# Optimization experiments

Hardware: AMD Instinct MI355X
Metric: run time of the kernel (lower is better)

The kernel has to match this reference:

```python
import jax, jax.numpy as jnp
import numpy as np

MAX_SEQ = 1024
NUM_HEADS = 16
NUM_KV_HEADS = 4
HEAD_DIM = 128
HIDDEN = 2048
GROUPS = NUM_HEADS // NUM_KV_HEADS
EPS = 1e-6
THETA = 1000000.0
SCALE = 1.0 / (HEAD_DIM ** 0.5)
POS = 512
B = 32


def setup_inputs() -> dict:
    key = jax.random.key(0)
    ks = jax.random.split(key, 8)
    x = jax.random.normal(ks[0], (B, 1, HIDDEN), dtype=jnp.float32)
    position = jnp.full((1,), float(POS), dtype=jnp.float32)
    mask = jnp.where(jnp.arange(MAX_SEQ) <= POS, 0.0, -1e9).astype(jnp.float32).reshape(1, 1, 1, MAX_SEQ)
    k_cache = jax.random.normal(ks[1], (B, NUM_KV_HEADS, MAX_SEQ, HEAD_DIM), dtype=jnp.float32)
    v_cache = jax.random.normal(ks[2], (B, NUM_KV_HEADS, MAX_SEQ, HEAD_DIM), dtype=jnp.float32)
    onehot = jnp.zeros((1, 1, MAX_SEQ, 1), dtype=jnp.float32).at[0, 0, POS, 0].set(1.0)
    wq = jax.random.normal(ks[3], (NUM_HEADS * HEAD_DIM, HIDDEN), dtype=jnp.float32) * 0.02
    wk = jax.random.normal(ks[4], (NUM_KV_HEADS * HEAD_DIM, HIDDEN), dtype=jnp.float32) * 0.02
    wv = jax.random.normal(ks[5], (NUM_KV_HEADS * HEAD_DIM, HIDDEN), dtype=jnp.float32) * 0.02
    wo = jax.random.normal(ks[6], (HIDDEN, NUM_HEADS * HEAD_DIM), dtype=jnp.float32) * 0.02
    q_norm_w = jnp.ones((HEAD_DIM,), dtype=jnp.float32)
    k_norm_w = jnp.ones((HEAD_DIM,), dtype=jnp.float32)
    return {"x": x, "position": position, "mask": mask, "k_cache": k_cache, "v_cache": v_cache,
            "onehot": onehot, "wq": wq, "wk": wk, "wv": wv, "wo": wo,
            "q_norm_w": q_norm_w, "k_norm_w": k_norm_w}


def _rmsnorm(t, w):
    tf = t.astype(jnp.float32)
    norm = jax.lax.rsqrt(jnp.mean(tf * tf, axis=-1, keepdims=True) + EPS)
    return (tf * norm * w).astype(t.dtype)


def _rope(t, position):
    half = HEAD_DIM // 2
    inv_freq = 1.0 / (THETA ** (jnp.arange(half, dtype=jnp.float32) / half))
    freqs = position * inv_freq  # [half]
    cos_v = jnp.cos(freqs).reshape(1, 1, 1, half)
    sin_v = jnp.sin(freqs).reshape(1, 1, 1, half)
    x1, x2 = t[..., :half], t[..., half:]
    return jnp.concatenate([x1 * cos_v - x2 * sin_v, x2 * cos_v + x1 * sin_v], axis=-1)


def reference(x, position, mask, k_cache, v_cache, onehot, wq, wk, wv, wo, q_norm_w, k_norm_w):
    Bsz, T, _ = x.shape
    # projections -> [B, heads, T, head_dim]
    q = (x @ wq.T).reshape(Bsz, T, NUM_HEADS, HEAD_DIM).transpose(0, 2, 1, 3)
    k = (x @ wk.T).reshape(Bsz, T, NUM_KV_HEADS, HEAD_DIM).transpose(0, 2, 1, 3)
    v = (x @ wv.T).reshape(Bsz, T, NUM_KV_HEADS, HEAD_DIM).transpose(0, 2, 1, 3)
    q = _rope(_rmsnorm(q, q_norm_w), position)
    k = _rope(_rmsnorm(k, k_norm_w), position)
    # functional one-hot cache update (in-place mul_/add_ in torch)
    kc = k_cache * (1.0 - onehot) + k * onehot  # [B, kvH, MAX_SEQ, hd]
    vc = v_cache * (1.0 - onehot) + v * onehot
    # GQA attention without materializing duplicated K/V: group the query heads
    qg = q.reshape(Bsz, NUM_KV_HEADS, GROUPS, T, HEAD_DIM)
    attn = jnp.einsum('bkgtd,bksd->bkgts', qg, kc) * SCALE  # [B,kvH,G,T,S]
    attn = attn + mask  # mask broadcasts over [*,*,*,T,S]
    attn = jax.nn.softmax(attn, axis=-1)
    out = jnp.einsum('bkgts,bksd->bkgtd', attn, vc)
    out = out.reshape(Bsz, NUM_HEADS, T, HEAD_DIM).transpose(0, 2, 1, 3).reshape(Bsz, T, NUM_HEADS * HEAD_DIM)
    return out @ wo.T
```

## Files before the change

### kernel.cpp

```cpp
#include <hip/hip_runtime.h>
#include <math.h>

#define MAX_SEQ   1024
#define NUM_HEADS 16
#define NUM_KV    4
#define HEAD_DIM  128
#define HIDDEN    2048
#define GROUPS    4
#define EPS       1e-6f
#define THETA     1000000.0f
#define SCALE     0.08838834764831845f
#define NSPLIT    8

#define QBUF  0
#define KBUF  65536
#define VBUF  81920
#define AOUT  98304
#define ARENA 163840

__device__ __forceinline__ void gemv_body(
    const float* __restrict__ W,
    const float* __restrict__ X,
    float* __restrict__ part,
    int RS, int grow0, int nkt)
{
    __shared__ float wt[128 * 68];
    __shared__ float xs[32 * 68];
    const int tid = threadIdx.x, lane = tid & 63, wave = tid >> 6;
    const int rg = tid >> 3, bg = tid & 7;
    const int rrow = wave * 4 + (lane >> 4);
    const int cf = (lane & 15) * 4;

    float acc[4][4];
    #pragma unroll
    for (int i = 0; i < 4; ++i)
        #pragma unroll
        for (int j = 0; j < 4; ++j) acc[i][j] = 0.f;

    for (int kt = 0; kt < nkt; ++kt) {
        const float* Wk = W + kt * 64;
        const float* Xk = X + kt * 64;
        #pragma unroll
        for (int it = 0; it < 8; ++it) {
            const int r = it * 16 + rrow;
            *(float4*)&wt[r * 68 + cf] = *(const float4*)(Wk + (size_t)r * HIDDEN + cf);
        }
        #pragma unroll
        for (int it = 0; it < 2; ++it) {
            const int b = it * 16 + rrow;
            *(float4*)&xs[b * 68 + cf] = *(const float4*)(Xk + (size_t)b * HIDDEN + cf);
        }
        __syncthreads();

        #pragma unroll
        for (int kk = 0; kk < 64; kk += 4) {
            float4 a[4], bb[4];
            #pragma unroll
            for (int i = 0; i < 4; ++i) a[i]  = *(const float4*)&wt[(rg * 4 + i) * 68 + kk];
            #pragma unroll
            for (int j = 0; j < 4; ++j) bb[j] = *(const float4*)&xs[(bg * 4 + j) * 68 + kk];
            #pragma unroll
            for (int i = 0; i < 4; ++i)
                #pragma unroll
                for (int j = 0; j < 4; ++j)
                    acc[i][j] += a[i].x * bb[j].x + a[i].y * bb[j].y
                               + a[i].z * bb[j].z + a[i].w * bb[j].w;
        }
        __syncthreads();
    }

    #pragma unroll
    for (int j = 0; j < 4; ++j) {
        float4 o = make_float4(acc[0][j], acc[1][j], acc[2][j], acc[3][j]);
        *(float4*)(part + (size_t)(bg * 4 + j) * RS + grow0 + rg * 4) = o;
    }
}

__global__ __launch_bounds__(256) void gemv_qkv(
    const float* __restrict__ x, const float* __restrict__ wq,
    const float* __restrict__ wk, const float* __restrict__ wv,
    float* __restrict__ ws)
{
    const int mt = blockIdx.x >> 3;
    const int ks = blockIdx.x & 7;
    const float* W;
    if (mt < 16)      W = wq + (size_t)mt * 128 * HIDDEN;
    else if (mt < 20) W = wk + (size_t)(mt - 16) * 128 * HIDDEN;
    else              W = wv + (size_t)(mt - 20) * 128 * HIDDEN;
    const int k0 = ks * 256;
    float* part = ws + ARENA + (size_t)ks * 32 * 3072;
    gemv_body(W + k0, x + k0, part, 3072, mt * 128, 4);
}

__global__ __launch_bounds__(128) void qkv_post(
    const float* __restrict__ position, const float* __restrict__ qnw,
    const float* __restrict__ knw, float* __restrict__ ws)
{
    const int blk = blockIdx.x;
    const int b = blk / 24, h = blk % 24;
    const int d = threadIdx.x, lane = d & 63, wave = d >> 6;
    const int grow = h * 128 + d;

    float v = 0.f;
    #pragma unroll
    for (int s = 0; s < NSPLIT; ++s)
        v += ws[ARENA + (size_t)(s * 32 + b) * 3072 + grow];

    if (h >= 20) {
        ws[VBUF + (size_t)(b * NUM_KV + (h - 20)) * HEAD_DIM + d] = v;
        return;
    }

    __shared__ float red[2];
    __shared__ float vl[128];
    vl[d] = v;
    float t2 = v * v;
    #pragma unroll
    for (int off = 32; off; off >>= 1) t2 += __shfl_xor(t2, off);
    if (lane == 0) red[wave] = t2;
    __syncthreads();

    if (d < 64) {
        const float norm = rsqrtf((red[0] + red[1]) * (1.0f / HEAD_DIM) + EPS);
        const float* nw = (h < 16) ? qnw : knw;
        float n1 = vl[d]      * norm * nw[d];
        float n2 = vl[d + 64] * norm * nw[d + 64];
        const float p = position[0];
        float invf = __powf(THETA, -(float)d * (1.0f / 64.0f));
        float f = p * invf, s, c;
        __sincosf(f, &s, &c);
        float* outp = (h < 16)
            ? ws + QBUF + (size_t)(b * NUM_HEADS + h) * HEAD_DIM
            : ws + KBUF + (size_t)(b * NUM_KV + (h - 16)) * HEAD_DIM;
        outp[d]      = n1 * c - n2 * s;
        outp[d + 64] = n2 * c + n1 * s;
    }
}

__global__ __launch_bounds__(256) void attn_kernel(
    const float* __restrict__ kcache, const float* __restrict__ vcache,
    const float* __restrict__ position, float* __restrict__ ws)
{
    const int blk = blockIdx.x;
    const int split = blk & (NSPLIT - 1);
    const int bk = blk >> 3;
    const int tid = threadIdx.x, lane = tid & 63, wave = tid >> 6;
    const int half = lane >> 5, li = lane & 31;
    const int b = bk >> 2, kv = bk & 3;
    const int pos = (int)position[0];

    const int chunk = (pos + NSPLIT) / NSPLIT;
    const int s0 = split * chunk;
    const int s1 = min(s0 + chunk, pos + 1);

    const float* qb = ws + QBUF + ((size_t)b * NUM_HEADS + kv * GROUPS) * HEAD_DIM;
    float4 q4[4];
    #pragma unroll
    for (int g = 0; g < 4; ++g)
        q4[g] = ((const float4*)(qb + g * HEAD_DIM))[li];

    const float* kc = kcache + (size_t)bk * MAX_SEQ * HEAD_DIM;
    const float* vc = vcache + (size_t)bk * MAX_SEQ * HEAD_DIM;
    const float* knew = ws + KBUF + (size_t)bk * HEAD_DIM;
    const float* vnew = ws + VBUF + (size_t)bk * HEAD_DIM;

    float m[4], l[4]; float4 acc[4];
    #pragma unroll
    for (int g = 0; g < 4; ++g) {
        m[g] = -1e30f; l[g] = 0.f;
        acc[g] = make_float4(0.f, 0.f, 0.f, 0.f);
    }

    for (int t = s0 + wave * 2 + half; t < s1; t += 16) {
        const int tb = t + 8;
        const bool vb = (tb < s1);
        const int tbc = vb ? tb : t;
        const float4* kpa = (const float4*)((t   == pos) ? knew : kc + (size_t)t   * HEAD_DIM);
        const float4* kpb = (const float4*)((tbc == pos) ? knew : kc + (size_t)tbc * HEAD_DIM);
        const float4* vpa = (const float4*)((t   == pos) ? vnew : vc + (size_t)t   * HEAD_DIM);
        const float4* vpb = (const float4*)((tbc == pos) ? vnew : vc + (size_t)tbc * HEAD_DIM);
        float4 ka = kpa[li], kb = kpb[li];
        float4 va = vpa[li], vb4 = vpb[li];

        float sa[4], sb[4];
        #pragma unroll
        for (int g = 0; g < 4; ++g) {
            sa[g] = q4[g].x * ka.x + q4[g].y * ka.y + q4[g].z * ka.z + q4[g].w * ka.w;
            sb[g] = q4[g].x * kb.x + q4[g].y * kb.y + q4[g].z * kb.z + q4[g].w * kb.w;
        }
        #pragma unroll
        for (int off = 16; off; off >>= 1) {
            #pragma unroll
            for (int g = 0; g < 4; ++g) {
                sa[g] += __shfl_xor(sa[g], off);
                sb[g] += __shfl_xor(sb[g], off);
            }
        }
        #pragma unroll
        for (int g = 0; g < 4; ++g) {
            float sga = sa[g] * SCALE;
            float sgb = vb ? sb[g] * SCALE : -1e30f;
            float mn  = fmaxf(m[g], fmaxf(sga, sgb));
            float alpha = __expf(m[g] - mn);
            float pa = __expf(sga - mn);
            float pb = vb ? __expf(sgb - mn) : 0.f;
            l[g] = l[g] * alpha + pa + pb;
            acc[g].x = acc[g].x * alpha + pa * va.x + pb * vb4.x;
            acc[g].y = acc[g].y * alpha + pa * va.y + pb * vb4.y;
            acc[g].z = acc[g].z * alpha + pa * va.z + pb * vb4.z;
            acc[g].w = acc[g].w * alpha + pa * va.w + pb * vb4.w;
            m[g] = mn;
        }
    }

    __shared__ float sm[8][4], sl[8][4];
    __shared__ float4 sacc[8][4][32];
    const int st = wave * 2 + half;
    #pragma unroll
    for (int g = 0; g < 4; ++g) {
        if (li == 0) { sm[st][g] = m[g]; sl[st][g] = l[g]; }
        sacc[st][g][li] = acc[g];
    }
    __syncthreads();

    float* part = ws + ARENA + (size_t)blk * 4 * 130;
    if (tid < HEAD_DIM) {
        const int d = tid;
        #pragma unroll
        for (int g = 0; g < 4; ++g) {
            float M = -1e30f;
            #pragma unroll
            for (int s = 0; s < 8; ++s) M = fmaxf(M, sm[s][g]);
            float L = 0.f, A = 0.f;
            #pragma unroll
            for (int s = 0; s < 8; ++s) {
                float e = __expf(sm[s][g] - M);
                L += sl[s][g] * e;
                A += ((const float*)&sacc[s][g][0])[d] * e;
            }
            part[g * 130 + d] = A;
            if (d == 0) { part[g * 130 + 128] = M; part[g * 130 + 129] = L; }
        }
    }
}

__global__ __launch_bounds__(128) void comb_kernel(float* __restrict__ ws)
{
    const int blk = blockIdx.x;
    const int b = blk >> 4, h = blk & 15;
    const int kv = h >> 2, g = h & 3;
    const int d = threadIdx.x;
    const float* base = ws + ARENA + ((size_t)(b * NUM_KV + kv) * NSPLIT) * 4 * 130 + g * 130;

    float ms[NSPLIT], ls[NSPLIT];
    float M = -1e30f;
    #pragma unroll
    for (int s = 0; s < NSPLIT; ++s) {
        ms[s] = base[s * 520 + 128];
        ls[s] = base[s * 520 + 129];
        M = fmaxf(M, ms[s]);
    }
    float L = 0.f, A = 0.f;
    #pragma unroll
    for (int s = 0; s < NSPLIT; ++s) {
        float e = __expf(ms[s] - M);
        L += ls[s] * e;
        A += base[s * 520 + d] * e;
    }
    ws[AOUT + (size_t)b * HIDDEN + h * HEAD_DIM + d] = A / L;
}

__global__ __launch_bounds__(256) void gemv_wo(
    const float* __restrict__ wo, float* __restrict__ ws)
{
    const int mt = blockIdx.x >> 4;
    const int ks = blockIdx.x & 15;
    const int k0 = ks * 128;
    float* part = ws + ARENA + (size_t)ks * 32 * 2048;
    gemv_body(wo + (size_t)mt * 128 * HIDDEN + k0, ws + AOUT + k0,
              part, 2048, mt * 128, 2);
}

__global__ __launch_bounds__(256) void ocomb(
    const float* __restrict__ ws, float* __restrict__ out)
{
    const int idx = blockIdx.x * 256 + threadIdx.x;
    const int b = idx >> 9, r4 = (idx & 511) * 4;
    float4 s = make_float4(0.f, 0.f, 0.f, 0.f);
    #pragma unroll
    for (int k = 0; k < 16; ++k) {
        float4 t = *(const float4*)(ws + ARENA + (size_t)(k * 32 + b) * 2048 + r4);
        s.x += t.x; s.y += t.y; s.z += t.z; s.w += t.w;
    }
    *(float4*)(out + (size_t)b * HIDDEN + r4) = s;
}

extern "C" void kernel_launch(void* const* d_in, const int* in_sizes, int n_in,
                              void* d_out, int out_size, void* d_ws, size_t ws_size,
                              hipStream_t stream) {
    const float* x        = (const float*)d_in[0];
    const float* position = (const float*)d_in[1];
    const float* kcache   = (const float*)d_in[3];
    const float* vcache   = (const float*)d_in[4];
    const float* wq       = (const float*)d_in[6];
    const float* wk       = (const float*)d_in[7];
    const float* wv       = (const float*)d_in[8];
    const float* wo       = (const float*)d_in[9];
    const float* qnw      = (const float*)d_in[10];
    const float* knw      = (const float*)d_in[11];
    float* ws  = (float*)d_ws;
    float* out = (float*)d_out;

    gemv_qkv<<<24 * 8, 256, 0, stream>>>(x, wq, wk, wv, ws);
    qkv_post<<<32 * 24, 128, 0, stream>>>(position, qnw, knw, ws);
    attn_kernel<<<32 * NUM_KV * NSPLIT, 256, 0, stream>>>(kcache, vcache, position, ws);
    comb_kernel<<<32 * NUM_HEADS, 128, 0, stream>>>(ws);
    gemv_wo<<<16 * 16, 256, 0, stream>>>(wo, ws);
    ocomb<<<64, 256, 0, stream>>>(ws, out);
}
```

Before: 218.9 us.

## Double-buffer GEMV weight tiles with register prefetch and smaller K tile

The shared GEMV body now uses two LDS buffers with a 32-wide K tile. The next tile's weights and activations are loaded into registers before computing on the current tile, so global load latency overlaps with the FMAs. The row mapping changes to a strided i*32+rg layout, so the output stores become scalar and no longer float4. This adds an extra barrier per iteration and halves the work per tile, which may offset the latency hiding.

```diff
diff --git a/kernel.cpp b/kernel.cpp
--- a/kernel.cpp
+++ b/kernel.cpp
@@ -11,6 +11,7 @@
 #define THETA     1000000.0f
 #define SCALE     0.08838834764831845f
 #define NSPLIT    8
+#define KT        32
 
 #define QBUF  0
 #define KBUF  65536
@@ -24,12 +25,36 @@
     float* __restrict__ part,
     int RS, int grow0, int nkt)
 {
-    __shared__ float wt[128 * 68];
-    __shared__ float xs[32 * 68];
-    const int tid = threadIdx.x, lane = tid & 63, wave = tid >> 6;
+    __shared__ float wt[2][128 * 36];
+    __shared__ float xs[2][32 * 36];
+    const int tid = threadIdx.x;
     const int rg = tid >> 3, bg = tid & 7;
-    const int rrow = wave * 4 + (lane >> 4);
-    const int cf = (lane & 15) * 4;
+    const int sr = tid >> 3, sc = (tid & 7) * 4;
+
+    float4 wreg[4];
+    float4 xreg;
+
+    #define ISSUE(kt_) do {                                                   \
+        const float* Wk_ = W + (kt_) * KT;                                    \
+        const float* Xk_ = X + (kt_) * KT;                                    \
+        _Pragma("unroll")                                                     \
+        for (int it = 0; it < 4; ++it) {                                      \
+            const int lin = it * 256 + tid;                                   \
+            const int r_ = lin >> 3, c_ = (lin & 7) * 4;                      \
+            wreg[it] = *(const float4*)(Wk_ + (size_t)r_ * HIDDEN + c_);      \
+        }                                                                     \
+        xreg = *(const float4*)(Xk_ + (size_t)sr * HIDDEN + sc);              \
+    } while (0)
+
+    #define COMMIT(buf_) do {                                                 \
+        _Pragma("unroll")                                                     \
+        for (int it = 0; it < 4; ++it) {                                      \
+            const int lin = it * 256 + tid;                                   \
+            const int r_ = lin >> 3, c_ = (lin & 7) * 4;                      \
+            *(float4*)&wt[buf_][r_ * 36 + c_] = wreg[it];                     \
+        }                                                                     \
+        *(float4*)&xs[buf_][sr * 36 + sc] = xreg;                             \
+    } while (0)
 
     float acc[4][4];
     #pragma unroll
@@ -37,28 +62,22 @@
         #pragma unroll
         for (int j = 0; j < 4; ++j) acc[i][j] = 0.f;
 
+    ISSUE(0); COMMIT(0);
+    __syncthreads();
+
     for (int kt = 0; kt < nkt; ++kt) {
-        const float* Wk = W + kt * 64;
-        const float* Xk = X + kt * 64;
-        #pragma unroll
-        for (int it = 0; it < 8; ++it) {
-            const int r = it * 16 + rrow;
-            *(float4*)&wt[r * 68 + cf] = *(const float4*)(Wk + (size_t)r * HIDDEN + cf);
-        }
-        #pragma unroll
-        for (int it = 0; it < 2; ++it) {
-            const int b = it * 16 + rrow;
-            *(float4*)&xs[b * 68 + cf] = *(const float4*)(Xk + (size_t)b * HIDDEN + cf);
-        }
-        __syncthreads();
-
-        #pragma unroll
-        for (int kk = 0; kk < 64; kk += 4) {
+        const int cur = kt & 1, nxt = cur ^ 1;
+        if (kt + 1 < nkt) ISSUE(kt + 1);
+
+        #pragma unroll
+        for (int kk = 0; kk < KT; kk += 4) {
             float4 a[4], bb[4];
             #pragma unroll
-            for (int i = 0; i < 4; ++i) a[i]  = *(const float4*)&wt[(rg * 4 + i) * 68 + kk];
-            #pragma unroll
-            for (int j = 0; j < 4; ++j) bb[j] = *(const float4*)&xs[(bg * 4 + j) * 68 + kk];
+            for (int i = 0; i < 4; ++i)
+                a[i] = *(const float4*)&wt[cur][(i * 32 + rg) * 36 + kk];
+            #pragma unroll
+            for (int j = 0; j < 4; ++j)
+                bb[j] = *(const float4*)&xs[cur][(j * 8 + bg) * 36 + kk];
             #pragma unroll
             for (int i = 0; i < 4; ++i)
                 #pragma unroll
@@ -67,13 +86,16 @@
                                + a[i].z * bb[j].z + a[i].w * bb[j].w;
         }
         __syncthreads();
-    }
-
-    #pragma unroll
-    for (int j = 0; j < 4; ++j) {
-        float4 o = make_float4(acc[0][j], acc[1][j], acc[2][j], acc[3][j]);
-        *(float4*)(part + (size_t)(bg * 4 + j) * RS + grow0 + rg * 4) = o;
-    }
+        if (kt + 1 < nkt) { COMMIT(nxt); __syncthreads(); }
+    }
+
+    #pragma unroll
+    for (int j = 0; j < 4; ++j)
+        #pragma unroll
+        for (int i = 0; i < 4; ++i)
+            part[(size_t)(j * 8 + bg) * RS + grow0 + i * 32 + rg] = acc[i][j];
+    #undef ISSUE
+    #undef COMMIT
 }
 
 __global__ __launch_bounds__(256) void gemv_qkv(
@@ -89,7 +111,7 @@
     else              W = wv + (size_t)(mt - 20) * 128 * HIDDEN;
     const int k0 = ks * 256;
     float* part = ws + ARENA + (size_t)ks * 32 * 3072;
-    gemv_body(W + k0, x + k0, part, 3072, mt * 128, 4);
+    gemv_body(W + k0, x + k0, part, 3072, mt * 128, 8);
 }
 
 __global__ __launch_bounds__(128) void qkv_post(
@@ -104,7 +126,7 @@
     float v = 0.f;
     #pragma unroll
     for (int s = 0; s < NSPLIT; ++s)
-        v += ws[ARENA + (size_t)(s * 32 + b) * 3072 + grow];
+        v += ws[ARENA + (size_t)s * 32 * 3072 + (size_t)b * 3072 + grow];
 
     if (h >= 20) {
         ws[VBUF + (size_t)(b * NUM_KV + (h - 20)) * HEAD_DIM + d] = v;
@@ -252,19 +274,14 @@
     const int d = threadIdx.x;
     const float* base = ws + ARENA + ((size_t)(b * NUM_KV + kv) * NSPLIT) * 4 * 130 + g * 130;
 
-    float ms[NSPLIT], ls[NSPLIT];
     float M = -1e30f;
     #pragma unroll
+    for (int s = 0; s < NSPLIT; ++s) M = fmaxf(M, base[s * 520 + 128]);
+    float L = 0.f, A = 0.f;
+    #pragma unroll
     for (int s = 0; s < NSPLIT; ++s) {
-        ms[s] = base[s * 520 + 128];
-        ls[s] = base[s * 520 + 129];
-        M = fmaxf(M, ms[s]);
-    }
-    float L = 0.f, A = 0.f;
-    #pragma unroll
-    for (int s = 0; s < NSPLIT; ++s) {
-        float e = __expf(ms[s] - M);
-        L += ls[s] * e;
+        float e = __expf(base[s * 520 + 128] - M);
+        L += base[s * 520 + 129] * e;
         A += base[s * 520 + d] * e;
     }
     ws[AOUT + (size_t)b * HIDDEN + h * HEAD_DIM + d] = A / L;
@@ -278,7 +295,7 @@
     const int k0 = ks * 128;
     float* part = ws + ARENA + (size_t)ks * 32 * 2048;
     gemv_body(wo + (size_t)mt * 128 * HIDDEN + k0, ws + AOUT + k0,
-              part, 2048, mt * 128, 2);
+              part, 2048, mt * 128, 4);
 }
 
 __global__ __launch_bounds__(256) void ocomb(
@@ -289,7 +306,7 @@
     float4 s = make_float4(0.f, 0.f, 0.f, 0.f);
     #pragma unroll
     for (int k = 0; k < 16; ++k) {
-        float4 t = *(const float4*)(ws + ARENA + (size_t)(k * 32 + b) * 2048 + r4);
+        float4 t = *(const float4*)(ws + ARENA + (size_t)k * 32 * 2048 + (size_t)b * 2048 + r4);
         s.x += t.x; s.y += t.y; s.z += t.z; s.w += t.w;
     }
     *(float4*)(out + (size_t)b * HIDDEN + r4) = s;
```

Measured after the change: 225.1 us. 2.8% more time.
